# Kernel optimization log

Hardware: AMD Instinct MI355X
Metric: run time of the kernel (lower is better)

The kernel has to match this reference:

```python
import jax, jax.numpy as jnp
import numpy as np

NUM_HEADS = 16
PAD_TAIL = 128  # last PAD_TAIL positions are padded


def setup_inputs() -> dict:
    key = jax.random.key(0)
    k1, k2, k3 = jax.random.split(key, 3)
    B, N, C = 2, 2048, 1024
    x = jax.random.normal(k1, (B, N, C), dtype=jnp.float32)
    # tail padding: True = padded (masked out), matching torch bool padding_mask
    padding_mask = jnp.broadcast_to(jnp.arange(N) >= (N - PAD_TAIL), (B, N))
    w_qkv = jax.random.normal(k2, (3 * C, C), dtype=jnp.float32) * (C ** -0.5)
    w_proj = jax.random.normal(k3, (C, C), dtype=jnp.float32) * (C ** -0.5)
    b_proj = jnp.zeros((C,), dtype=jnp.float32)
    return {
        "x": x,
        "padding_mask": padding_mask,
        "causal_start": 16,
        "w_qkv": w_qkv,
        "w_proj": w_proj,
        "b_proj": b_proj,
    }


def reference(x, padding_mask, causal_start, w_qkv, w_proj, b_proj):
    B, N, C = x.shape
    H = NUM_HEADS
    hd = C // H
    # qkv projection (no bias), split into q,k,v of shape (B,H,N,hd)
    qkv = (x @ w_qkv.T).reshape(B, N, 3, H, hd)
    qkv = jnp.transpose(qkv, (2, 0, 3, 1, 4))  # (3,B,H,N,hd)
    q, k, v = qkv[0], qkv[1], qkv[2]
    present = jnp.stack([k, v])  # (2,B,H,N,hd)

    # allowed[b,q,k] = not padded(key) AND (k <= q OR k < causal_start)
    rows = jnp.arange(N)[:, None]
    cols = jnp.arange(N)[None, :]
    causal_ok = (cols <= rows) | (cols < causal_start)  # (N,N)
    allowed = (~padding_mask)[:, None, None, :] & causal_ok[None, None, :, :]  # (B,1,N,N)

    # SDPA default scale = head_dim**-0.5 (module's self.scale equals this when qk_scale=None)
    scale = hd ** -0.5
    scores = jnp.einsum("bhqd,bhkd->bhqk", q, k) * scale  # (B,H,N,N)
    neg = jnp.finfo(scores.dtype).min
    scores = jnp.where(allowed, scores, neg)
    attn = jax.nn.softmax(scores, axis=-1)
    out = jnp.einsum("bhqk,bhkd->bhqd", attn, v)  # (B,H,N,hd)
    out = jnp.transpose(out, (0, 2, 1, 3)).reshape(B, N, C)
    out = out @ w_proj.T + b_proj
    return (out, present)
```

## Files before the change

### kernel.cpp

```cpp
#include <hip/hip_runtime.h>


typedef unsigned short ushort_t;
typedef short short8 __attribute__((ext_vector_type(8)));
typedef float floatx4 __attribute__((ext_vector_type(4)));
typedef unsigned short ushort4v __attribute__((ext_vector_type(4)));

#define MFMA16(a, b, c) __builtin_amdgcn_mfma_f32_16x16x32_bf16(a, b, c, 0, 0, 0)

__device__ __forceinline__ ushort_t f2bf(float f) {
  unsigned int u = __float_as_uint(f);
  u += 0x7fffu + ((u >> 16) & 1u);
  return (ushort_t)(u >> 16);
}

__device__ __forceinline__ void gl_lds16(const ushort_t* g, ushort_t* l) {
  __builtin_amdgcn_global_load_lds(
      (const __attribute__((address_space(1))) void*)g,
      (__attribute__((address_space(3))) void*)l, 16, 0, 0);
}

__global__ __launch_bounds__(256) void cvt_all_kernel(
    const float* __restrict__ x, const float* __restrict__ wq,
    const float* __restrict__ wp, ushort_t* __restrict__ xb,
    ushort_t* __restrict__ wqb, ushort_t* __restrict__ wpb) {
  int i = (blockIdx.x * 256 + threadIdx.x) * 4;
  const float* s;
  ushort_t* d;
  int off;
  if (i < (4 << 20)) {
    s = x; d = xb; off = i;
  } else if (i < (7 << 20)) {
    s = wq; d = wqb; off = i - (4 << 20);
  } else {
    s = wp; d = wpb; off = i - (7 << 20);
  }
  float4 v = *(const float4*)(s + off);
  ushort4v o;
  o.x = f2bf(v.x); o.y = f2bf(v.y); o.z = f2bf(v.z); o.w = f2bf(v.w);
  *(ushort4v*)(d + off) = o;
}

template <int EPI>
__global__ __launch_bounds__(256) void gemm_bt(
    const ushort_t* __restrict__ A, const ushort_t* __restrict__ Bm,
    int K, int TNC,
    float* __restrict__ outf, float* __restrict__ present,
    ushort_t* __restrict__ q_ws, ushort_t* __restrict__ k_ws,
    ushort_t* __restrict__ vT_ws, const float* __restrict__ b_proj) {
  __shared__ __align__(16) ushort_t As[2 * 128 * 32];
  __shared__ __align__(16) ushort_t Bs[2 * 64 * 32];
  const int tid = threadIdx.x;
  const int wave = tid >> 6, lane = tid & 63;
  const int quad = lane >> 4, l16 = lane & 15;
  const int wm = wave >> 1, wn = wave & 1;
  const int xcd = blockIdx.x & 7;
  const int loc = blockIdx.x >> 3;
  const int tm = (xcd >> 1) * 8 + (loc & 7);
  const int tn = (xcd & 1) * TNC + (loc >> 3);

  const int r0 = tid >> 2, c0 = (tid & 3) * 8;
  const int r1 = r0 + 64;
  const ushort_t* a0 = A + (size_t)(tm * 128 + r0) * K + c0;
  const ushort_t* a1 = A + (size_t)(tm * 128 + r1) * K + c0;
  const ushort_t* b0 = Bm + (size_t)(tn * 64 + r0) * K + c0;
  ushort_t* lA0 = As + tid * 8;
  ushort_t* lA1 = As + (tid + 256) * 8;
  ushort_t* lB0 = Bs + tid * 8;

  auto stage = [&](int bsel, int k0) {
    gl_lds16(a0 + k0, lA0 + bsel * 4096);
    gl_lds16(a1 + k0, lA1 + bsel * 4096);
    gl_lds16(b0 + k0, lB0 + bsel * 2048);
  };

  floatx4 acc[4][2] = {};

  stage(0, 0);
  __syncthreads();
  int buf = 0;

  for (int k0 = 0; k0 < K; k0 += 32) {
    if (k0 + 32 < K) stage(buf ^ 1, k0 + 32);
    const ushort_t* as = As + buf * 4096;
    const ushort_t* bs = Bs + buf * 2048;
    short8 af[4], bfr[2];
#pragma unroll
    for (int mi = 0; mi < 4; ++mi)
      af[mi] = *(const short8*)(as + (wm * 64 + mi * 16 + l16) * 32 + quad * 8);
#pragma unroll
    for (int ni = 0; ni < 2; ++ni)
      bfr[ni] = *(const short8*)(bs + (wn * 32 + ni * 16 + l16) * 32 + quad * 8);
#pragma unroll
    for (int mi = 0; mi < 4; ++mi)
#pragma unroll
      for (int ni = 0; ni < 2; ++ni)
        acc[mi][ni] = MFMA16(af[mi], bfr[ni], acc[mi][ni]);
    __syncthreads();
    buf ^= 1;
  }

#pragma unroll
  for (int mi = 0; mi < 4; ++mi) {
#pragma unroll
    for (int ni = 0; ni < 2; ++ni) {
      const int gm0 = tm * 128 + wm * 64 + mi * 16 + quad * 4;
      const int gn = tn * 64 + wn * 32 + ni * 16 + l16;
      if constexpr (EPI == 0) {
        const int b = gm0 >> 11, pos0 = gm0 & 2047;
        const int which = gn >> 10, rem = gn & 1023;
        const int h = rem >> 6, d = rem & 63;
        const size_t hb = (size_t)(b * 16 + h);
        if (which == 0) {
#pragma unroll
          for (int r = 0; r < 4; ++r)
            q_ws[(hb * 2048 + pos0 + r) * 64 + d] =
                f2bf(acc[mi][ni][r] * 0.1803368867f);
        } else if (which == 1) {
#pragma unroll
          for (int r = 0; r < 4; ++r) {
            size_t pk = (hb * 2048 + pos0 + r) * 64 + d;
            present[pk] = acc[mi][ni][r];
            k_ws[pk] = f2bf(acc[mi][ni][r]);
          }
        } else {
#pragma unroll
          for (int r = 0; r < 4; ++r)
            present[((size_t)((2 + b) * 16 + h) * 2048 + pos0 + r) * 64 + d] =
                acc[mi][ni][r];
          ushort4v pk4;
          pk4.x = f2bf(acc[mi][ni][0]); pk4.y = f2bf(acc[mi][ni][1]);
          pk4.z = f2bf(acc[mi][ni][2]); pk4.w = f2bf(acc[mi][ni][3]);
          *(ushort4v*)(vT_ws + (hb * 64 + d) * 2048 + pos0) = pk4;
        }
      } else {
#pragma unroll
        for (int r = 0; r < 4; ++r)
          outf[(size_t)(gm0 + r) * 1024 + gn] = acc[mi][ni][r] + b_proj[gn];
      }
    }
  }
}

__global__ __launch_bounds__(256) void attn_kernel(
    const ushort_t* __restrict__ qw, const ushort_t* __restrict__ kw,
    const ushort_t* __restrict__ vtw, ushort_t* __restrict__ attn_out,
    const int* __restrict__ cs_ptr) {
  __shared__ __align__(16) ushort_t Ks[2 * 64 * 64];
  __shared__ __align__(16) ushort_t Vs[2 * 64 * 64];
  const int tid = threadIdx.x;
  const int lane = tid & 63;
  const int wave = tid >> 6;
  const int quad = lane >> 4, l16 = lane & 15;

  const int bid = blockIdx.x;
  const int bh = bid & 31;
  const int j = bid >> 5;
  const int i = j & 7, g = j >> 3;
  const int qt = (g == 0) ? i : (g == 1) ? (31 - i) : (g == 2) ? (8 + i) : (23 - i);
  const int b = bh >> 4, h = bh & 15;
  const int cs = cs_ptr[0];
  const size_t headP = (size_t)(b * 16 + h) * 2048 * 64;

  int offk[2], offv[2];
#pragma unroll
  for (int s = 0; s < 2; ++s) {
    const int krow = s * 32 + (tid >> 3);
    const int f = ((krow >> 3) & 1) | ((krow & 3) << 1);
    offk[s] = krow * 64 + (((tid & 7) ^ f) << 3);
    const int vrow = s * 32 + (tid >> 3);
    const int vj = (tid & 7) ^ (vrow & 7);
    offv[s] = vrow * 2048 + vj * 8;
  }
  const ushort_t* kbase = kw + headP;
  const ushort_t* vbase = vtw + headP;
  ushort_t* lK = Ks + tid * 8;
  ushort_t* lV = Vs + tid * 8;

  const int kswz = ((l16 >> 2) & 1) | ((l16 & 3) << 1);
  const int vswz = l16 & 7;
  const int lrow = ((l16 >> 2) << 3) + (l16 & 3);

  int buf = 0;
  auto stage = [&](int bsel, int kt0) {
    ushort_t* dK = lK + bsel * 4096;
    ushort_t* dV = lV + bsel * 4096;
#pragma unroll
    for (int s = 0; s < 2; ++s)
      gl_lds16(kbase + (size_t)kt0 * 64 + offk[s], dK + s * 2048);
#pragma unroll
    for (int s = 0; s < 2; ++s)
      gl_lds16(vbase + kt0 + offv[s], dV + s * 2048);
  };

  const int q0 = qt * 64;
  const int wq0 = q0 + wave * 16;

  short8 qf[2];
  {
    const int qrow = wq0 + l16;
    qf[0] = *(const short8*)(qw + headP + (size_t)qrow * 64 + quad * 8);
    qf[1] = *(const short8*)(qw + headP + (size_t)qrow * 64 + 32 + quad * 8);
  }

  floatx4 OT[4] = {};
  float m_ = -1e30f, l_ = 0.f;

  const int kmax = min(1920, max(q0 + 64, cs));
  const int ntiles = (kmax + 63) >> 6;

  stage(0, 0);
  __syncthreads();

  for (int t = 0; t < ntiles; ++t) {
    const int kt0 = t << 6;
    if (t + 1 < ntiles) stage(buf ^ 1, kt0 + 64);

    const bool active = !(kt0 > wq0 + 15 && kt0 >= cs);
    if (active) {
      const ushort_t* kb = Ks + buf * 4096;

      floatx4 ST[4];
      __builtin_amdgcn_s_setprio(1);
#pragma unroll
      for (int ni = 0; ni < 4; ++ni) {
        const int nrow = ((ni & 1) << 5) + ((ni >> 1) << 2);
        const ushort_t* krow = kb + (nrow + lrow) * 64;
        short8 kf0 = *(const short8*)(krow + ((quad ^ kswz) << 3));
        short8 kf1 = *(const short8*)(krow + (((quad + 4) ^ kswz) << 3));
        floatx4 z = {};
        z = MFMA16(kf0, qf[0], z);
        ST[ni] = MFMA16(kf1, qf[1], z);
      }
      __builtin_amdgcn_s_setprio(0);

      if (kt0 + 63 > wq0) {
        const int qq = wq0 + l16;
#pragma unroll
        for (int ni = 0; ni < 4; ++ni) {
          const int kb0 = kt0 + ((ni & 1) << 5) + ((ni >> 1) << 2) + (quad << 3);
#pragma unroll
          for (int r = 0; r < 4; ++r) {
            const int k = kb0 + r;
            if (!(k <= qq || k < cs)) ST[ni][r] = -1e30f;
          }
        }
      }

      float mt;
      {
        float t0 = fmaxf(fmaxf(ST[0][0], ST[0][1]), ST[0][2]);
        float t1 = fmaxf(fmaxf(ST[0][3], ST[1][0]), ST[1][1]);
        float t2 = fmaxf(fmaxf(ST[1][2], ST[1][3]), ST[2][0]);
        float t3 = fmaxf(fmaxf(ST[2][1], ST[2][2]), ST[2][3]);
        float t4 = fmaxf(fmaxf(ST[3][0], ST[3][1]), ST[3][2]);
        float u0 = fmaxf(fmaxf(t0, t1), t2);
        float u1 = fmaxf(fmaxf(t3, t4), ST[3][3]);
        mt = fmaxf(u0, u1);
      }
      mt = fmaxf(mt, __shfl_xor(mt, 16, 64));
      mt = fmaxf(mt, __shfl_xor(mt, 32, 64));
      if (!__all(mt <= m_ + 8.0f)) {
        const float mn = fmaxf(m_, mt);
        const float al = exp2f(m_ - mn);
        m_ = mn;
        l_ *= al;
#pragma unroll
        for (int di = 0; di < 4; ++di) OT[di] *= al;
      }
      float sub[4];
#pragma unroll
      for (int ni = 0; ni < 4; ++ni) {
        float p0 = exp2f(ST[ni][0] - m_);
        float p1 = exp2f(ST[ni][1] - m_);
        float p2 = exp2f(ST[ni][2] - m_);
        float p3 = exp2f(ST[ni][3] - m_);
        ST[ni][0] = p0; ST[ni][1] = p1; ST[ni][2] = p2; ST[ni][3] = p3;
        sub[ni] = (p0 + p1) + (p2 + p3);
      }
      l_ += (sub[0] + sub[1]) + (sub[2] + sub[3]);

      const ushort_t* vb = Vs + buf * 4096;
#pragma unroll
      for (int s = 0; s < 2; ++s) {
        int d0, d1, d2, d3;
        asm("v_cvt_pk_bf16_f32 %0, %1, %2" : "=v"(d0) : "v"(ST[s][0]), "v"(ST[s][1]));
        asm("v_cvt_pk_bf16_f32 %0, %1, %2" : "=v"(d1) : "v"(ST[s][2]), "v"(ST[s][3]));
        asm("v_cvt_pk_bf16_f32 %0, %1, %2" : "=v"(d2) : "v"(ST[s + 2][0]), "v"(ST[s + 2][1]));
        asm("v_cvt_pk_bf16_f32 %0, %1, %2" : "=v"(d3) : "v"(ST[s + 2][2]), "v"(ST[s + 2][3]));
        union { int i[4]; short8 v; } u;
        u.i[0] = d0; u.i[1] = d1; u.i[2] = d2; u.i[3] = d3;
        const short8 pb = u.v;
        __builtin_amdgcn_s_setprio(1);
#pragma unroll
        for (int di = 0; di < 4; ++di) {
          const ushort_t* vrow = vb + (di * 16 + l16) * 64;
          short8 vf = *(const short8*)(vrow + ((((s << 2) + quad) ^ vswz) << 3));
          OT[di] = MFMA16(vf, pb, OT[di]);
        }
        __builtin_amdgcn_s_setprio(0);
      }
    }

    __syncthreads();
    buf ^= 1;
  }

  l_ += __shfl_xor(l_, 16, 64);
  l_ += __shfl_xor(l_, 32, 64);
  const float inv = 1.f / l_;
  const int qq = wq0 + l16;
#pragma unroll
  for (int di = 0; di < 4; ++di) {
    ushort4v o4;
    o4.x = f2bf(OT[di][0] * inv);
    o4.y = f2bf(OT[di][1] * inv);
    o4.z = f2bf(OT[di][2] * inv);
    o4.w = f2bf(OT[di][3] * inv);
    *(ushort4v*)(attn_out + ((size_t)(b * 2048 + qq)) * 1024 + h * 64 +
                 di * 16 + quad * 4) = o4;
  }
}

extern "C" void kernel_launch(void* const* d_in, const int* in_sizes, int n_in,
                              void* d_out, int out_size, void* d_ws, size_t ws_size,
                              hipStream_t stream) {
  const float* x      = (const float*)d_in[0];
  const int*   cs     = (const int*)d_in[2];
  const float* w_qkv  = (const float*)d_in[3];
  const float* w_proj = (const float*)d_in[4];
  const float* b_proj = (const float*)d_in[5];

  float* out     = (float*)d_out;
  float* present = out + (size_t)2 * 2048 * 1024;

  char* ws = (char*)d_ws;
  ushort_t* xb      = (ushort_t*)(ws);
  ushort_t* wqb     = (ushort_t*)(ws + ((size_t)8  << 20));
  ushort_t* wpb     = (ushort_t*)(ws + ((size_t)14 << 20));
  ushort_t* q_ws    = (ushort_t*)(ws + ((size_t)16 << 20));
  ushort_t* k_ws    = (ushort_t*)(ws + ((size_t)24 << 20));
  ushort_t* vT_ws   = (ushort_t*)(ws + ((size_t)32 << 20));
  ushort_t* attn_ws = (ushort_t*)(ws + ((size_t)40 << 20));

  cvt_all_kernel<<<8192, 256, 0, stream>>>(x, w_qkv, w_proj, xb, wqb, wpb);

  gemm_bt<0><<<1536, 256, 0, stream>>>(xb, wqb, 1024, 24,
                                       nullptr, present, q_ws, k_ws, vT_ws, nullptr);

  attn_kernel<<<1024, 256, 0, stream>>>(q_ws, k_ws, vT_ws, attn_ws, cs);

  gemm_bt<1><<<512, 256, 0, stream>>>(attn_ws, wpb, 1024, 8,
                                      out, nullptr, nullptr, nullptr, nullptr, b_proj);
}
```

Before: 198.5 us.

## Triple-buffer GEMM loads, widen QKV tile to 128, use raw v_exp in attention

The GEMM moves from a double-buffered to a triple-buffered LDS pipeline. Prefetch now runs two k-steps ahead, with explicit vmcnt waits and a single barrier per step. The QKV projection GEMM tile widens from 128x64 to 128x128 (half the blocks, more MFMAs per loaded A tile), which cuts A-operand reloads at the cost of more registers and LDS. The attention softmax swaps exp2f for the raw v_exp_f32 instruction to skip the library's range handling.

```diff
diff --git a/kernel.cpp b/kernel.cpp
--- a/kernel.cpp
+++ b/kernel.cpp
@@ -12,6 +12,12 @@
   unsigned int u = __float_as_uint(f);
   u += 0x7fffu + ((u >> 16) & 1u);
   return (ushort_t)(u >> 16);
+}
+
+__device__ __forceinline__ float fexp2(float x) {
+  float r;
+  asm("v_exp_f32 %0, %1" : "=v"(r) : "v"(x));
+  return r;
 }
 
 __device__ __forceinline__ void gl_lds16(const ushort_t* g, ushort_t* l) {
@@ -41,15 +47,18 @@
   *(ushort4v*)(d + off) = o;
 }
 
-template <int EPI>
+template <int EPI, int NT>
 __global__ __launch_bounds__(256) void gemm_bt(
     const ushort_t* __restrict__ A, const ushort_t* __restrict__ Bm,
     int K, int TNC,
     float* __restrict__ outf, float* __restrict__ present,
     ushort_t* __restrict__ q_ws, ushort_t* __restrict__ k_ws,
     ushort_t* __restrict__ vT_ws, const float* __restrict__ b_proj) {
-  __shared__ __align__(16) ushort_t As[2 * 128 * 32];
-  __shared__ __align__(16) ushort_t Bs[2 * 64 * 32];
+  constexpr int ABUF = 128 * 32;
+  constexpr int BBUF = NT * 32;
+  constexpr int BNF = NT / 32;
+  __shared__ __align__(16) ushort_t As[3 * ABUF];
+  __shared__ __align__(16) ushort_t Bs[3 * BBUF];
   const int tid = threadIdx.x;
   const int wave = tid >> 6, lane = tid & 63;
   const int quad = lane >> 4, l16 = lane & 15;
@@ -63,49 +72,69 @@
   const int r1 = r0 + 64;
   const ushort_t* a0 = A + (size_t)(tm * 128 + r0) * K + c0;
   const ushort_t* a1 = A + (size_t)(tm * 128 + r1) * K + c0;
-  const ushort_t* b0 = Bm + (size_t)(tn * 64 + r0) * K + c0;
+  const ushort_t* b0 = Bm + (size_t)(tn * NT + r0) * K + c0;
+  const ushort_t* b1 = (NT == 128) ? Bm + (size_t)(tn * NT + r1) * K + c0 : Bm;
   ushort_t* lA0 = As + tid * 8;
   ushort_t* lA1 = As + (tid + 256) * 8;
   ushort_t* lB0 = Bs + tid * 8;
+  ushort_t* lB1 = Bs + (tid + 256) * 8;
 
   auto stage = [&](int bsel, int k0) {
-    gl_lds16(a0 + k0, lA0 + bsel * 4096);
-    gl_lds16(a1 + k0, lA1 + bsel * 4096);
-    gl_lds16(b0 + k0, lB0 + bsel * 2048);
+    gl_lds16(a0 + k0, lA0 + bsel * ABUF);
+    gl_lds16(a1 + k0, lA1 + bsel * ABUF);
+    gl_lds16(b0 + k0, lB0 + bsel * BBUF);
+    if constexpr (NT == 128) gl_lds16(b1 + k0, lB1 + bsel * BBUF);
   };
 
-  floatx4 acc[4][2] = {};
+  floatx4 acc[4][BNF] = {};
 
   stage(0, 0);
-  __syncthreads();
-  int buf = 0;
-
+  stage(1, 32);
+  if constexpr (NT == 128) asm volatile("s_waitcnt vmcnt(4)" ::: "memory");
+  else                     asm volatile("s_waitcnt vmcnt(3)" ::: "memory");
+  asm volatile("" ::: "memory");
+  __builtin_amdgcn_s_barrier();
+  asm volatile("" ::: "memory");
+
+  int cur = 0, stg = 2;
   for (int k0 = 0; k0 < K; k0 += 32) {
-    if (k0 + 32 < K) stage(buf ^ 1, k0 + 32);
-    const ushort_t* as = As + buf * 4096;
-    const ushort_t* bs = Bs + buf * 2048;
-    short8 af[4], bfr[2];
+    if (k0 + 64 < K) stage(stg, k0 + 64);
+    const ushort_t* as = As + cur * ABUF;
+    const ushort_t* bs = Bs + cur * BBUF;
+    short8 af[4], bfr[BNF];
 #pragma unroll
     for (int mi = 0; mi < 4; ++mi)
       af[mi] = *(const short8*)(as + (wm * 64 + mi * 16 + l16) * 32 + quad * 8);
 #pragma unroll
-    for (int ni = 0; ni < 2; ++ni)
-      bfr[ni] = *(const short8*)(bs + (wn * 32 + ni * 16 + l16) * 32 + quad * 8);
+    for (int ni = 0; ni < BNF; ++ni)
+      bfr[ni] = *(const short8*)(bs + (wn * (NT / 2) + ni * 16 + l16) * 32 + quad * 8);
 #pragma unroll
     for (int mi = 0; mi < 4; ++mi)
 #pragma unroll
-      for (int ni = 0; ni < 2; ++ni)
+      for (int ni = 0; ni < BNF; ++ni)
         acc[mi][ni] = MFMA16(af[mi], bfr[ni], acc[mi][ni]);
-    __syncthreads();
-    buf ^= 1;
+
+    if (k0 + 32 < K) {
+      if (k0 + 64 < K) {
+        if constexpr (NT == 128) asm volatile("s_waitcnt vmcnt(4)" ::: "memory");
+        else                     asm volatile("s_waitcnt vmcnt(3)" ::: "memory");
+      } else {
+        asm volatile("s_waitcnt vmcnt(0)" ::: "memory");
+      }
+      asm volatile("" ::: "memory");
+      __builtin_amdgcn_s_barrier();
+      asm volatile("" ::: "memory");
+    }
+    cur = (cur == 2) ? 0 : cur + 1;
+    stg = (stg == 2) ? 0 : stg + 1;
   }
 
 #pragma unroll
   for (int mi = 0; mi < 4; ++mi) {
 #pragma unroll
-    for (int ni = 0; ni < 2; ++ni) {
+    for (int ni = 0; ni < BNF; ++ni) {
       const int gm0 = tm * 128 + wm * 64 + mi * 16 + quad * 4;
-      const int gn = tn * 64 + wn * 32 + ni * 16 + l16;
+      const int gn = tn * NT + wn * (NT / 2) + ni * 16 + l16;
       if constexpr (EPI == 0) {
         const int b = gm0 >> 11, pos0 = gm0 & 2047;
         const int which = gn >> 10, rem = gn & 1023;
@@ -262,7 +291,7 @@
       mt = fmaxf(mt, __shfl_xor(mt, 32, 64));
       if (!__all(mt <= m_ + 8.0f)) {
         const float mn = fmaxf(m_, mt);
-        const float al = exp2f(m_ - mn);
+        const float al = fexp2(m_ - mn);
         m_ = mn;
         l_ *= al;
 #pragma unroll
@@ -271,10 +300,10 @@
       float sub[4];
 #pragma unroll
       for (int ni = 0; ni < 4; ++ni) {
-        float p0 = exp2f(ST[ni][0] - m_);
-        float p1 = exp2f(ST[ni][1] - m_);
-        float p2 = exp2f(ST[ni][2] - m_);
-        float p3 = exp2f(ST[ni][3] - m_);
+        float p0 = fexp2(ST[ni][0] - m_);
+        float p1 = fexp2(ST[ni][1] - m_);
+        float p2 = fexp2(ST[ni][2] - m_);
+        float p3 = fexp2(ST[ni][3] - m_);
         ST[ni][0] = p0; ST[ni][1] = p1; ST[ni][2] = p2; ST[ni][3] = p3;
         sub[ni] = (p0 + p1) + (p2 + p3);
       }
@@ -345,11 +374,11 @@
 
   cvt_all_kernel<<<8192, 256, 0, stream>>>(x, w_qkv, w_proj, xb, wqb, wpb);
 
-  gemm_bt<0><<<1536, 256, 0, stream>>>(xb, wqb, 1024, 24,
-                                       nullptr, present, q_ws, k_ws, vT_ws, nullptr);
+  gemm_bt<0, 128><<<768, 256, 0, stream>>>(xb, wqb, 1024, 12,
+                                           nullptr, present, q_ws, k_ws, vT_ws, nullptr);
 
   attn_kernel<<<1024, 256, 0, stream>>>(q_ws, k_ws, vT_ws, attn_ws, cs);
 
-  gemm_bt<1><<<512, 256, 0, stream>>>(attn_ws, wpb, 1024, 8,
-                                      out, nullptr, nullptr, nullptr, nullptr, b_proj);
-}
+  gemm_bt<1, 64><<<512, 256, 0, stream>>>(attn_ws, wpb, 1024, 8,
+                                          out, nullptr, nullptr, nullptr, nullptr, b_proj);
+}
```

After: 217.5 us. 1.1x slower.
